# Optimization experiments

Hardware: AMD Instinct MI355X
Metric: run time of the kernel (lower is better)

Reference implementation:

```python
import jax, jax.numpy as jnp
import numpy as np

N, C, I, E = 4096, 128, 9, 10
IRREPS_OUT = [(1, 0), (3, 1)]          # (M = 2L+1, L) for target irreps 128x0e + 128x1o
PATHS = {0: (1, 2, 5), 1: (1, 3, 7)}   # (P1, P2, P3) CG path counts per output L


def setup_inputs() -> dict:
    key = jax.random.key(0)
    ks = jax.random.split(key, 32)
    inp = {}
    inp['node_feats'] = jax.random.normal(ks[0], (N, C, I), jnp.float32)
    out_dim = C * sum(m for m, _ in IRREPS_OUT)
    inp['sc'] = jax.random.normal(ks[1], (N, out_dim), jnp.float32)
    elem = jax.random.randint(ks[2], (N,), 0, E)
    inp['node_attrs'] = jax.nn.one_hot(elem, E, dtype=jnp.float32)
    i = 3
    for (M, L) in IRREPS_OUT:
        P1, P2, P3 = PATHS[L]
        # U tensors: fixed (non-learned) generalized CG basis; random stand-ins with correct shapes
        inp[f'U3_{L}'] = jax.random.normal(ks[i], (M, I, I, I, P3), jnp.float32) * 0.1; i += 1
        inp[f'U2_{L}'] = jax.random.normal(ks[i], (M, I, I, P2), jnp.float32) * 0.1; i += 1
        inp[f'U1_{L}'] = jax.random.normal(ks[i], (M, I, P1), jnp.float32) * 0.1; i += 1
        # element-indexed learned weights [E, P, C]
        inp[f'W3_{L}'] = jax.random.normal(ks[i], (E, P3, C), jnp.float32) / np.sqrt(P3); i += 1
        inp[f'W2_{L}'] = jax.random.normal(ks[i], (E, P2, C), jnp.float32) / np.sqrt(P2); i += 1
        inp[f'W1_{L}'] = jax.random.normal(ks[i], (E, P1, C), jnp.float32) / np.sqrt(P1); i += 1
        # equivariant Linear internal weight (per-irrep channel mixing)
        inp[f'Wlin_{L}'] = jax.random.normal(ks[i], (C, C), jnp.float32); i += 1
    return inp


def _symmetric_contract(x, y, U3, U2, U1, W3, W2, W1):
    """Correlation-3 symmetric CG contraction for one output irrep.
    x: [N,C,I] node feats, y: [N,E] one-hot element attrs. Returns [N,C,M]."""
    # per-node element-selected weights (gather via one-hot matmul): [N,P,C]
    w3 = jnp.einsum('ne,epc->npc', y, W3)
    w2 = jnp.einsum('ne,epc->npc', y, W2)
    w1 = jnp.einsum('ne,epc->npc', y, W1)
    # highest correlation: out[n,c,m,a,b] = sum_{i,p} U3[m,a,b,i,p] w3[n,p,c] x[n,c,i]
    xw = jnp.einsum('nci,npc->nipc', x, w3)            # [N,I,P3,C]
    out = jnp.einsum('mabip,nipc->ncmab', U3, xw)      # [N,C,M,I,I]  (largest intermediate)
    # correlation 2 term, then contract one irrep index with x
    out = out + jnp.einsum('mabp,npc->ncmab', U2, w2)
    out = jnp.einsum('ncmab,ncb->ncma', out, x)        # [N,C,M,I]
    # correlation 1 term, contract last irrep index
    out = out + jnp.einsum('map,npc->ncma', U1, w1)
    out = jnp.einsum('ncma,nca->ncm', out, x)          # [N,C,M]
    return out


def reference(node_feats, sc, node_attrs,
              U3_0, U2_0, U1_0, W3_0, W2_0, W1_0, Wlin_0,
              U3_1, U2_1, U1_1, W3_1, W2_1, W1_1, Wlin_1):
    params = {0: (U3_0, U2_0, U1_0, W3_0, W2_0, W1_0, Wlin_0),
              1: (U3_1, U2_1, U1_1, W3_1, W2_1, W1_1, Wlin_1)}
    inv_sqrt_c = 1.0 / np.sqrt(C)
    blocks = []
    for (M, L) in IRREPS_OUT:
        U3, U2, U1, W3, W2, W1, Wl = params[L]
        b = _symmetric_contract(node_feats, node_attrs, U3, U2, U1, W3, W2, W1)  # [N,C,M]
        b = jnp.einsum('ncm,cd->ndm', b, Wl) * inv_sqrt_c  # e3nn-style Linear, internal weights
        blocks.append(b.reshape(b.shape[0], -1))           # [N, C*M]
    out = jnp.concatenate(blocks, axis=-1)                 # [N, 512]
    return out + sc                                        # use_sc residual
```

## Files before the change

### kernel.cpp

```cpp
#include <hip/hip_runtime.h>

#define N_NODES 4096
#define C_CH    128
#define E_ELEM  10
#define NP      4736
#define TT      219
#define PSTRIDE (TT * 4)
#define MAXCHUNK 32
#define CHUNK_J  256

#define WS_CHE     256
#define WS_CHJ     512
#define WS_CHEND   768
#define WS_JLIST   1024
#define WS_ELEM    20480
#define WS_S31     53248
#define WS_S30     67136
#define WS_S21     70464
#define WS_S20     72128
#define WS_P       72704
#define WS_BOUT    4557824

__device__ __forceinline__ void t3_decode(int t, int& a, int& b, int& i) {
    int cnt = 0;
    for (int aa = 0; aa < 9; ++aa)
        for (int bb = aa; bb < 9; ++bb) {
            int len = 9 - bb;
            if (t < cnt + len) { a = aa; b = bb; i = bb + (t - cnt); return; }
            cnt += len;
        }
    a = b = i = 8;
}

__device__ __forceinline__ void t2_decode(int t, int& a, int& b) {
    int cnt = 0;
    for (int aa = 0; aa < 9; ++aa) {
        int len = 9 - aa;
        if (t < cnt + len) { a = aa; b = aa + (t - cnt); return; }
        cnt += len;
    }
    a = b = 8;
}

__global__ __launch_bounds__(256) void k_front(
    const float* __restrict__ attrs, int* __restrict__ elem,
    const float* __restrict__ U3_1, const float* __restrict__ U3_0,
    const float* __restrict__ U2_1, const float* __restrict__ U2_0,
    float* __restrict__ S31, float* __restrict__ S30,
    float* __restrict__ S21, float* __restrict__ S20) {
    int bid = blockIdx.x;
    if (bid >= 19) {
        int n = (bid - 19) * 256 + threadIdx.x;
        if (n >= N_NODES) return;
        const float* a = attrs + n * E_ELEM;
        float best = a[0];
        int e = 0;
#pragma unroll
        for (int k = 1; k < E_ELEM; ++k) {
            float v = a[k];
            if (v > best) { best = v; e = k; }
        }
        elem[n] = e;
        return;
    }
    int q = bid * 256 + threadIdx.x;
    if (q < 3465) {
        int m = q / 1155, r = q % 1155, t = r / 7, p = r % 7;
        int a, b, i;
        t3_decode(t, a, b, i);
#define U31(X, Y, Z) U3_1[((((m * 9 + (X)) * 9 + (Y)) * 9 + (Z)) * 7) + p]
        float s = U31(a, b, i);
        if (a == b && b == i) {}
        else if (a == b) s += U31(a, i, a) + U31(i, a, a);
        else if (b == i) s += U31(b, a, b) + U31(b, b, a);
        else s += U31(a, i, b) + U31(b, a, i) + U31(b, i, a) + U31(i, a, b) + U31(i, b, a);
#undef U31
        S31[q] = s;
        return;
    }
    q -= 3465;
    if (q < 825) {
        int t = q / 5, p = q % 5;
        int a, b, i;
        t3_decode(t, a, b, i);
#define U30(X, Y, Z) U3_0[((((X) * 9 + (Y)) * 9 + (Z)) * 5) + p]
        float s = U30(a, b, i);
        if (a == b && b == i) {}
        else if (a == b) s += U30(a, i, a) + U30(i, a, a);
        else if (b == i) s += U30(b, a, b) + U30(b, b, a);
        else s += U30(a, i, b) + U30(b, a, i) + U30(b, i, a) + U30(i, a, b) + U30(i, b, a);
#undef U30
        S30[q] = s;
        return;
    }
    q -= 825;
    if (q < 405) {
        int m = q / 135, r = q % 135, t = r / 3, p = r % 3;
        int a, b;
        t2_decode(t, a, b);
        float s = U2_1[(((m * 9 + a) * 9 + b) * 3) + p];
        if (a != b) s += U2_1[(((m * 9 + b) * 9 + a) * 3) + p];
        S21[q] = s;
        return;
    }
    q -= 405;
    if (q < 90) {
        int t = q / 2, p = q % 2;
        int a, b;
        t2_decode(t, a, b);
        float s = U2_0[((a * 9 + b) * 2) + p];
        if (a != b) s += U2_0[((b * 9 + a) * 2) + p];
        S20[q] = s;
    }
}

__global__ __launch_bounds__(1024) void k_sortfold(
    const int* __restrict__ elem, int* __restrict__ jlist,
    int* __restrict__ chE, int* __restrict__ chJ, int* __restrict__ chEnd,
    const float* __restrict__ S31, const float* __restrict__ S30,
    const float* __restrict__ S21, const float* __restrict__ S20,
    const float* __restrict__ U1_1, const float* __restrict__ U1_0,
    const float* __restrict__ W3_1, const float* __restrict__ W3_0,
    const float* __restrict__ W2_1, const float* __restrict__ W2_0,
    const float* __restrict__ W1_1, const float* __restrict__ W1_0,
    float* __restrict__ P) {
    const int bid = blockIdx.x;
    const int tid = threadIdx.x;
    if (bid == 0) {
        __shared__ int h[E_ELEM];
        __shared__ int cur[E_ELEM];
        if (tid < E_ELEM) h[tid] = 0;
        __syncthreads();
        for (int n = tid; n < N_NODES; n += 1024) atomicAdd(&h[elem[n]], 1);
        for (int p = tid; p < NP; p += 1024) jlist[p] = -1;
        __syncthreads();
        if (tid == 0) {
            int ps[E_ELEM + 1];
            int s = 0;
            for (int e = 0; e < E_ELEM; ++e) {
                ps[e] = s;
                cur[e] = s;
                s += ((h[e] + 63) >> 6) << 6;
            }
            ps[E_ELEM] = s;
            int ci = 0;
            for (int e = 0; e < E_ELEM; ++e) {
                for (int ofs = ps[e]; ofs < ps[e + 1]; ofs += CHUNK_J) {
                    chE[ci] = e;
                    chJ[ci] = ofs;
                    chEnd[ci] = ps[e + 1];
                    ++ci;
                }
            }
            for (; ci < MAXCHUNK; ++ci) chE[ci] = -1;
        }
        __syncthreads();
        for (int n = tid; n < N_NODES; n += 1024) {
            int e = elem[n];
            int pos = atomicAdd(&cur[e], 1);
            jlist[pos] = n;
        }
        return;
    }
    int fb = bid - 1;
    int e = fb >> 7;
    int c = fb & 127;
    float* Pout = P + (size_t)fb * PSTRIDE;
    for (int q = tid; q < PSTRIDE; q += 1024) {
        int t = q >> 2, m = q & 3;
        float v;
        if (t < 9) {
            int a = t;
            v = (m == 0) ? U1_0[a] * W1_0[e * C_CH + c]
                         : U1_1[(m - 1) * 9 + a] * W1_1[e * C_CH + c];
        } else if (t < 54) {
            int t2 = t - 9;
            float s = 0.f;
            if (m == 0) {
#pragma unroll
                for (int p = 0; p < 2; ++p)
                    s = fmaf(S20[t2 * 2 + p], W2_0[(e * 2 + p) * C_CH + c], s);
            } else {
#pragma unroll
                for (int p = 0; p < 3; ++p)
                    s = fmaf(S21[((m - 1) * 45 + t2) * 3 + p], W2_1[(e * 3 + p) * C_CH + c], s);
            }
            v = s;
        } else {
            int t3 = t - 54;
            float s = 0.f;
            if (m == 0) {
#pragma unroll
                for (int p = 0; p < 5; ++p)
                    s = fmaf(S30[t3 * 5 + p], W3_0[(e * 5 + p) * C_CH + c], s);
            } else {
#pragma unroll
                for (int p = 0; p < 7; ++p)
                    s = fmaf(S31[((m - 1) * 165 + t3) * 7 + p], W3_1[(e * 7 + p) * C_CH + c], s);
            }
            v = s;
        }
        Pout[q] = v;
    }
}

__device__ __forceinline__ void poly_eval1(const float* __restrict__ sP,
                                           const float (&xv)[9], float (&acc)[4]) {
    const float* p1 = sP;
    const float* p2 = sP + 9 * 4;
    const float* p3 = sP + 54 * 4;
    int i2 = 0, i3 = 0;
#pragma unroll
    for (int a = 0; a < 9; ++a) {
        float4 q1 = *(const float4*)(p1 + a * 4);
        float xa = xv[a];
        acc[0] = fmaf(q1.x, xa, acc[0]);
        acc[1] = fmaf(q1.y, xa, acc[1]);
        acc[2] = fmaf(q1.z, xa, acc[2]);
        acc[3] = fmaf(q1.w, xa, acc[3]);
        __builtin_amdgcn_sched_barrier(0);
#pragma unroll
        for (int b = a; b < 9; ++b) {
            float4 q2 = *(const float4*)(p2 + i2 * 4);
            ++i2;
            float m2 = xv[a] * xv[b];
            acc[0] = fmaf(q2.x, m2, acc[0]);
            acc[1] = fmaf(q2.y, m2, acc[1]);
            acc[2] = fmaf(q2.z, m2, acc[2]);
            acc[3] = fmaf(q2.w, m2, acc[3]);
#pragma unroll
            for (int i = b; i < 9; ++i) {
                float4 q3 = *(const float4*)(p3 + i3 * 4);
                ++i3;
                float m3 = m2 * xv[i];
                acc[0] = fmaf(q3.x, m3, acc[0]);
                acc[1] = fmaf(q3.y, m3, acc[1]);
                acc[2] = fmaf(q3.z, m3, acc[2]);
                acc[3] = fmaf(q3.w, m3, acc[3]);
            }
            __builtin_amdgcn_sched_barrier(0);
        }
    }
}

__global__ __launch_bounds__(256) void k_poly(
    const float* __restrict__ x, const int* __restrict__ jlist,
    const int* __restrict__ chE, const int* __restrict__ chJ,
    const int* __restrict__ chEnd, const float* __restrict__ P,
    float* __restrict__ bout) {
    int ci = blockIdx.y;
    int e = chE[ci];
    if (e < 0) return;
    e = __builtin_amdgcn_readfirstlane(e);
    int c = blockIdx.x;
    const float* __restrict__ Pg = P + (size_t)(e * C_CH + c) * PSTRIDE;

    const int end = chEnd[ci];
    const int j = chJ[ci] + threadIdx.x;
    if (j >= end) return;
    const int n = jlist[j];
    if (n < 0) return;

    float xv[9];
    const float* px = x + ((size_t)n * C_CH + c) * 9;
#pragma unroll
    for (int i = 0; i < 9; ++i) xv[i] = px[i];
    float acc[4] = {};
    poly_eval1(Pg, xv, acc);
#pragma unroll
    for (int m = 0; m < 4; ++m) bout[(size_t)(c * 4 + m) * NP + j] = acc[m];
}

__global__ __launch_bounds__(256) void k_linear(
    const float* __restrict__ bout, const int* __restrict__ jlist,
    const float* __restrict__ Wl0, const float* __restrict__ Wl1,
    const float* __restrict__ sc, float* __restrict__ out) {
    const int s  = blockIdx.y >> 2;
    const int dg = blockIdx.y & 3;
    const int jj = threadIdx.x & 63;
    const int wv = threadIdx.x >> 6;
    const int dbase = __builtin_amdgcn_readfirstlane(dg * 32 + wv * 8);
    const int j = blockIdx.x * 64 + jj;
    const float* __restrict__ Wl = (s == 0) ? Wl0 : Wl1;
    const float* __restrict__ brow = bout + (size_t)s * NP + j;

    float acc[8];
#pragma unroll
    for (int k = 0; k < 8; ++k) acc[k] = 0.f;

#pragma unroll 1
    for (int cc0 = 0; cc0 < C_CH; cc0 += 32) {
        float bv[32];
#pragma unroll
        for (int t = 0; t < 32; ++t)
            bv[t] = brow[(size_t)(cc0 + t) * 4 * NP];
#pragma unroll
        for (int t = 0; t < 32; ++t) {
            const float* wrow = Wl + (cc0 + t) * C_CH + dbase;
#pragma unroll
            for (int k = 0; k < 8; ++k) acc[k] = fmaf(bv[t], wrow[k], acc[k]);
        }
    }

    const int n = jlist[j];
    if (n < 0) return;
    const float inv = 0.08838834764831845f;
#pragma unroll
    for (int k = 0; k < 8; ++k) {
        int d = dbase + k;
        int col = (s == 0) ? d : (128 + d * 3 + (s - 1));
        out[n * 512 + col] = fmaf(acc[k], inv, sc[n * 512 + col]);
    }
}

extern "C" void kernel_launch(void* const* d_in, const int* in_sizes, int n_in,
                              void* d_out, int out_size, void* d_ws, size_t ws_size,
                              hipStream_t stream) {
    const float* x     = (const float*)d_in[0];
    const float* sc    = (const float*)d_in[1];
    const float* attrs = (const float*)d_in[2];
    const float* U3_0 = (const float*)d_in[3];
    const float* U2_0 = (const float*)d_in[4];
    const float* U1_0 = (const float*)d_in[5];
    const float* W3_0 = (const float*)d_in[6];
    const float* W2_0 = (const float*)d_in[7];
    const float* W1_0 = (const float*)d_in[8];
    const float* Wl0  = (const float*)d_in[9];
    const float* U3_1 = (const float*)d_in[10];
    const float* U2_1 = (const float*)d_in[11];
    const float* U1_1 = (const float*)d_in[12];
    const float* W3_1 = (const float*)d_in[13];
    const float* W2_1 = (const float*)d_in[14];
    const float* W1_1 = (const float*)d_in[15];
    const float* Wl1  = (const float*)d_in[16];

    char* ws = (char*)d_ws;
    int* chE     = (int*)(ws + WS_CHE);
    int* chJ     = (int*)(ws + WS_CHJ);
    int* chEnd   = (int*)(ws + WS_CHEND);
    int* jlist   = (int*)(ws + WS_JLIST);
    int* elem    = (int*)(ws + WS_ELEM);
    float* S31   = (float*)(ws + WS_S31);
    float* S30   = (float*)(ws + WS_S30);
    float* S21   = (float*)(ws + WS_S21);
    float* S20   = (float*)(ws + WS_S20);
    float* P     = (float*)(ws + WS_P);
    float* bout  = (float*)(ws + WS_BOUT);

    k_front<<<35, 256, 0, stream>>>(attrs, elem, U3_1, U3_0, U2_1, U2_0,
                                    S31, S30, S21, S20);
    k_sortfold<<<1281, 1024, 0, stream>>>(elem, jlist, chE, chJ, chEnd,
                                          S31, S30, S21, S20, U1_1, U1_0,
                                          W3_1, W3_0, W2_1, W2_0, W1_1, W1_0, P);
    k_poly<<<dim3(128, MAXCHUNK), 256, 0, stream>>>(x, jlist, chE, chJ, chEnd,
                                                    P, bout);
    k_linear<<<dim3(NP / 64, 16), 256, 0, stream>>>(bout, jlist, Wl0, Wl1, sc,
                                                    (float*)d_out);
}
```

Baseline: 77.00 us.

## Parallelize element bucketing across blocks with per-block histograms

Per-block element histograms are now computed in k_front, and the counting-sort scatter in k_sortfold is spread over 16 blocks using prefix offsets instead of one 1024-thread block. The fold blocks drop to 256 threads, and one extra block writes chunk metadata and fills only the padding slots with -1. Chunk ends now point to the real element count rather than the padded end. The sched_barrier hints in the polynomial evaluation are also removed, so the compiler is free to reorder those FMAs. The aim is to shorten the serial sort phase, at the cost of an extra prefix-sum pass per block.

```diff
diff --git a/kernel.cpp b/kernel.cpp
--- a/kernel.cpp
+++ b/kernel.cpp
@@ -4,6 +4,7 @@
 #define C_CH    128
 #define E_ELEM  10
 #define NP      4736
+#define NB      16
 #define TT      219
 #define PSTRIDE (TT * 4)
 #define MAXCHUNK 32
@@ -14,6 +15,7 @@
 #define WS_CHEND   768
 #define WS_JLIST   1024
 #define WS_ELEM    20480
+#define WS_BCNT    36864
 #define WS_S31     53248
 #define WS_S30     67136
 #define WS_S21     70464
@@ -44,14 +46,19 @@
 
 __global__ __launch_bounds__(256) void k_front(
     const float* __restrict__ attrs, int* __restrict__ elem,
+    int* __restrict__ bcnt,
     const float* __restrict__ U3_1, const float* __restrict__ U3_0,
     const float* __restrict__ U2_1, const float* __restrict__ U2_0,
     float* __restrict__ S31, float* __restrict__ S30,
     float* __restrict__ S21, float* __restrict__ S20) {
     int bid = blockIdx.x;
+    int tid = threadIdx.x;
     if (bid >= 19) {
-        int n = (bid - 19) * 256 + threadIdx.x;
-        if (n >= N_NODES) return;
+        __shared__ int h[E_ELEM];
+        if (tid < E_ELEM) h[tid] = 0;
+        __syncthreads();
+        int b = bid - 19;
+        int n = b * 256 + tid;
         const float* a = attrs + n * E_ELEM;
         float best = a[0];
         int e = 0;
@@ -61,9 +68,12 @@
             if (v > best) { best = v; e = k; }
         }
         elem[n] = e;
-        return;
-    }
-    int q = bid * 256 + threadIdx.x;
+        atomicAdd(&h[e], 1);
+        __syncthreads();
+        if (tid < E_ELEM) bcnt[b * E_ELEM + tid] = h[tid];
+        return;
+    }
+    int q = bid * 256 + tid;
     if (q < 3465) {
         int m = q / 1155, r = q % 1155, t = r / 7, p = r % 7;
         int a, b, i;
@@ -114,8 +124,32 @@
     }
 }
 
-__global__ __launch_bounds__(1024) void k_sortfold(
-    const int* __restrict__ elem, int* __restrict__ jlist,
+__device__ __forceinline__ void scan_bcnt(const int* __restrict__ bcnt,
+                                          int tid, int (&s_bc)[NB * E_ELEM],
+                                          int (&s_cnt)[E_ELEM], int (&s_ps)[E_ELEM + 1]) {
+    if (tid < NB * E_ELEM) s_bc[tid] = bcnt[tid];
+    __syncthreads();
+    if (tid < E_ELEM) {
+        int c = 0;
+#pragma unroll
+        for (int b = 0; b < NB; ++b) c += s_bc[b * E_ELEM + tid];
+        s_cnt[tid] = c;
+    }
+    __syncthreads();
+    if (tid == 0) {
+        int s = 0;
+        for (int e = 0; e < E_ELEM; ++e) {
+            s_ps[e] = s;
+            s += ((s_cnt[e] + 63) >> 6) << 6;
+        }
+        s_ps[E_ELEM] = s;
+    }
+    __syncthreads();
+}
+
+__global__ __launch_bounds__(256) void k_sortfold(
+    const int* __restrict__ elem, const int* __restrict__ bcnt,
+    int* __restrict__ jlist,
     int* __restrict__ chE, int* __restrict__ chJ, int* __restrict__ chEnd,
     const float* __restrict__ S31, const float* __restrict__ S30,
     const float* __restrict__ S21, const float* __restrict__ S20,
@@ -126,47 +160,60 @@
     float* __restrict__ P) {
     const int bid = blockIdx.x;
     const int tid = threadIdx.x;
-    if (bid == 0) {
-        __shared__ int h[E_ELEM];
+    if (bid < NB) {
+        __shared__ int s_bc[NB * E_ELEM];
+        __shared__ int s_cnt[E_ELEM];
+        __shared__ int s_ps[E_ELEM + 1];
         __shared__ int cur[E_ELEM];
-        if (tid < E_ELEM) h[tid] = 0;
+        scan_bcnt(bcnt, tid, s_bc, s_cnt, s_ps);
+        if (tid < E_ELEM) {
+            int off = s_ps[tid];
+            for (int b = 0; b < bid; ++b) off += s_bc[b * E_ELEM + tid];
+            cur[tid] = off;
+        }
         __syncthreads();
-        for (int n = tid; n < N_NODES; n += 1024) atomicAdd(&h[elem[n]], 1);
-        for (int p = tid; p < NP; p += 1024) jlist[p] = -1;
-        __syncthreads();
+        int n = bid * 256 + tid;
+        int e = elem[n];
+        int pos = atomicAdd(&cur[e], 1);
+        jlist[pos] = n;
+        return;
+    }
+    if (bid == NB) {
+        __shared__ int s_bc[NB * E_ELEM];
+        __shared__ int s_cnt[E_ELEM];
+        __shared__ int s_ps[E_ELEM + 1];
+        scan_bcnt(bcnt, tid, s_bc, s_cnt, s_ps);
         if (tid == 0) {
-            int ps[E_ELEM + 1];
-            int s = 0;
-            for (int e = 0; e < E_ELEM; ++e) {
-                ps[e] = s;
-                cur[e] = s;
-                s += ((h[e] + 63) >> 6) << 6;
-            }
-            ps[E_ELEM] = s;
             int ci = 0;
             for (int e = 0; e < E_ELEM; ++e) {
-                for (int ofs = ps[e]; ofs < ps[e + 1]; ofs += CHUNK_J) {
+                int base = s_ps[e], pend = s_ps[e + 1];
+                int end = base + s_cnt[e];
+                for (int ofs = base; ofs < pend; ofs += CHUNK_J) {
                     chE[ci] = e;
                     chJ[ci] = ofs;
-                    chEnd[ci] = ps[e + 1];
+                    chEnd[ci] = end;
                     ++ci;
                 }
             }
             for (; ci < MAXCHUNK; ++ci) chE[ci] = -1;
         }
-        __syncthreads();
-        for (int n = tid; n < N_NODES; n += 1024) {
-            int e = elem[n];
-            int pos = atomicAdd(&cur[e], 1);
-            jlist[pos] = n;
-        }
-        return;
-    }
-    int fb = bid - 1;
+        for (int j = tid; j < NP; j += 256) {
+            bool pad = j >= s_ps[E_ELEM];
+            if (!pad) {
+#pragma unroll
+                for (int e = 0; e < E_ELEM; ++e)
+                    if (j >= s_ps[e] && j < s_ps[e + 1] && j >= s_ps[e] + s_cnt[e])
+                        pad = true;
+            }
+            if (pad) jlist[j] = -1;
+        }
+        return;
+    }
+    int fb = bid - NB - 1;
     int e = fb >> 7;
     int c = fb & 127;
     float* Pout = P + (size_t)fb * PSTRIDE;
-    for (int q = tid; q < PSTRIDE; q += 1024) {
+    for (int q = tid; q < PSTRIDE; q += 256) {
         int t = q >> 2, m = q & 3;
         float v;
         if (t < 9) {
@@ -218,7 +265,6 @@
         acc[1] = fmaf(q1.y, xa, acc[1]);
         acc[2] = fmaf(q1.z, xa, acc[2]);
         acc[3] = fmaf(q1.w, xa, acc[3]);
-        __builtin_amdgcn_sched_barrier(0);
 #pragma unroll
         for (int b = a; b < 9; ++b) {
             float4 q2 = *(const float4*)(p2 + i2 * 4);
@@ -238,7 +284,6 @@
                 acc[2] = fmaf(q3.z, m3, acc[2]);
                 acc[3] = fmaf(q3.w, m3, acc[3]);
             }
-            __builtin_amdgcn_sched_barrier(0);
         }
     }
 }
@@ -340,6 +385,7 @@
     int* chEnd   = (int*)(ws + WS_CHEND);
     int* jlist   = (int*)(ws + WS_JLIST);
     int* elem    = (int*)(ws + WS_ELEM);
+    int* bcnt    = (int*)(ws + WS_BCNT);
     float* S31   = (float*)(ws + WS_S31);
     float* S30   = (float*)(ws + WS_S30);
     float* S21   = (float*)(ws + WS_S21);
@@ -347,11 +393,12 @@
     float* P     = (float*)(ws + WS_P);
     float* bout  = (float*)(ws + WS_BOUT);
 
-    k_front<<<35, 256, 0, stream>>>(attrs, elem, U3_1, U3_0, U2_1, U2_0,
+    k_front<<<35, 256, 0, stream>>>(attrs, elem, bcnt, U3_1, U3_0, U2_1, U2_0,
                                     S31, S30, S21, S20);
-    k_sortfold<<<1281, 1024, 0, stream>>>(elem, jlist, chE, chJ, chEnd,
-                                          S31, S30, S21, S20, U1_1, U1_0,
-                                          W3_1, W3_0, W2_1, W2_0, W1_1, W1_0, P);
+    k_sortfold<<<NB + 1 + 1280, 256, 0, stream>>>(
+        elem, bcnt, jlist, chE, chJ, chEnd,
+        S31, S30, S21, S20, U1_1, U1_0,
+        W3_1, W3_0, W2_1, W2_0, W1_1, W1_0, P);
     k_poly<<<dim3(128, MAXCHUNK), 256, 0, stream>>>(x, jlist, chE, chJ, chEnd,
                                                     P, bout);
     k_linear<<<dim3(NP / 64, 16), 256, 0, stream>>>(bout, jlist, Wl0, Wl1, sc,
```

New measurement: 78.17 us. Within noise of the previous version (+1.5%).
